# Performance work log

Measured on AMD Instinct MI355X. Metric: run time of the kernel, lower is better.

## Reference

```python
import jax, jax.numpy as jnp
import numpy as np

SMOOTH_COEF = 0.025
FLOOR = 1e-06
B, T, C = 64, 4096, 128


def setup_inputs() -> dict:
    key = jax.random.key(0)
    k1, = jax.random.split(key, 1)
    inputs = jax.random.uniform(k1, (B, T, C), dtype=jnp.float32)  # nonneg spectrogram-like
    alpha = jnp.full((C,), 0.98, dtype=jnp.float32)
    delta = jnp.full((C,), 2.0, dtype=jnp.float32)
    root = jnp.full((C,), 2.0, dtype=jnp.float32)
    return {"inputs": inputs, "alpha": alpha, "delta": delta, "root": root}


def _ema(x, s):
    # m_t = s*x_t + (1-s)*m_{t-1}, with h_{-1} = x_0 => m_0 = x_0.
    # Linear recurrence via associative scan: pairs (a_t, b_t), m_t = a_t*m_{t-1} + b_t.
    Bn, Tn, Cn = x.shape
    a = jnp.full((Tn,), 1.0 - s, dtype=x.dtype).at[0].set(0.0)
    a = jnp.broadcast_to(a[None, :, None], x.shape)
    b = (s * x).at[:, 0, :].set(x[:, 0, :])

    def comb(c1, c2):
        a1, b1 = c1
        a2, b2 = c2
        return (a1 * a2, a2 * b1 + b2)

    _, m = jax.lax.associative_scan(comb, (a, b), axis=1)
    return m


def reference(inputs, alpha, delta, root):
    alpha_c = jnp.minimum(alpha, 1.0)          # [C]
    root_c = jnp.maximum(root, 1.0)            # [C]
    m = _ema(inputs, SMOOTH_COEF)              # [B,T,C] EMA smoother
    one_over_root = 1.0 / root_c
    term1 = jnp.power(FLOOR + m, alpha_c)
    term2 = jnp.power(inputs / term1 + delta, one_over_root)
    term3 = jnp.power(delta, one_over_root)
    return term2 - term3
```

## Files before the change

### kernel.cpp

```cpp
#include <hip/hip_runtime.h>


constexpr int Bn = 64, Tn = 4096, Cn = 128;
constexpr int NC = 64;
constexpr int Lc = Tn / NC;
constexpr float SC  = 0.025f;
constexpr float OMS = 1.0f - SC;
constexpr float FLOORV = 1e-6f;

__host__ __device__ constexpr float chunk_decay() {
    float a = 1.0f;
    for (int i = 0; i < Lc; ++i) a *= OMS;
    return a;
}
constexpr float ACH = chunk_decay();


__global__ __launch_bounds__(256) void k_partial(const float* __restrict__ x,
                                                 float* __restrict__ endv) {
    int gid   = blockIdx.x * 256 + threadIdx.x;
    int cg    = gid & 31;
    int chunk = (gid >> 5) & (NC - 1);
    int b     = gid >> 11;

    const float4* xp = (const float4*)x + (size_t)(b * Tn + chunk * Lc) * (Cn / 4) + cg;

    float4 v = xp[0];
    float4 m;
    if (chunk == 0) {
        m = v;
    } else {
        m.x = SC * v.x; m.y = SC * v.y; m.z = SC * v.z; m.w = SC * v.w;
    }
#pragma unroll 8
    for (int t = 1; t < Lc; ++t) {
        v = xp[(size_t)t * (Cn / 4)];
        m.x = fmaf(OMS, m.x, SC * v.x);
        m.y = fmaf(OMS, m.y, SC * v.y);
        m.z = fmaf(OMS, m.z, SC * v.z);
        m.w = fmaf(OMS, m.w, SC * v.w);
    }
    float4* ep = (float4*)endv + (size_t)(b * NC + chunk) * (Cn / 4) + cg;
    *ep = m;
}

__global__ __launch_bounds__(256) void k_scan(float* __restrict__ endv) {
    int gid = blockIdx.x * 256 + threadIdx.x;
    int cg  = gid & 31;
    int b   = gid >> 5;
    float4* p = (float4*)endv + (size_t)b * NC * (Cn / 4) + cg;
    float4 acc = {0.f, 0.f, 0.f, 0.f};
    for (int j = 0; j < NC; ++j) {
        float4 e = p[(size_t)j * (Cn / 4)];
        p[(size_t)j * (Cn / 4)] = acc;
        acc.x = fmaf(ACH, acc.x, e.x);
        acc.y = fmaf(ACH, acc.y, e.y);
        acc.z = fmaf(ACH, acc.z, e.z);
        acc.w = fmaf(ACH, acc.w, e.w);
    }
}

__device__ __forceinline__ float pcen_elem(float x, float m, float al, float dl,
                                           float oor, float t3) {
    float lg   = log2f(FLOORV + m);
    float inv1 = exp2f(-al * lg);
    float base = fmaf(x, inv1, dl);
    return exp2f(oor * log2f(base)) - t3;
}

__global__ __launch_bounds__(256) void k_final(const float* __restrict__ x,
                                               const float* __restrict__ alpha,
                                               const float* __restrict__ delta,
                                               const float* __restrict__ root,
                                               const float* __restrict__ inc,
                                               float* __restrict__ out) {
    int gid   = blockIdx.x * 256 + threadIdx.x;
    int cg    = gid & 31;
    int chunk = (gid >> 5) & (NC - 1);
    int b     = gid >> 11;
    int c0    = cg * 4;

    float4 al = *(const float4*)(alpha + c0);
    float4 dl = *(const float4*)(delta + c0);
    float4 rt = *(const float4*)(root + c0);
    al.x = fminf(al.x, 1.f); al.y = fminf(al.y, 1.f); al.z = fminf(al.z, 1.f); al.w = fminf(al.w, 1.f);
    rt.x = fmaxf(rt.x, 1.f); rt.y = fmaxf(rt.y, 1.f); rt.z = fmaxf(rt.z, 1.f); rt.w = fmaxf(rt.w, 1.f);
    float4 oor = {1.f / rt.x, 1.f / rt.y, 1.f / rt.z, 1.f / rt.w};
    float4 t3  = {exp2f(oor.x * log2f(dl.x)), exp2f(oor.y * log2f(dl.y)),
                  exp2f(oor.z * log2f(dl.z)), exp2f(oor.w * log2f(dl.w))};

    size_t xoff = (size_t)(b * Tn + chunk * Lc) * (Cn / 4) + cg;
    const float4* xp = (const float4*)x + xoff;
    float4*       op = (float4*)out + xoff;

    float4 m = *((const float4*)inc + (size_t)(b * NC + chunk) * (Cn / 4) + cg);

    float4 v = xp[0];
    if (chunk == 0) {
        m = v;
    } else {
        m.x = fmaf(OMS, m.x, SC * v.x);
        m.y = fmaf(OMS, m.y, SC * v.y);
        m.z = fmaf(OMS, m.z, SC * v.z);
        m.w = fmaf(OMS, m.w, SC * v.w);
    }
    float4 o;
    o.x = pcen_elem(v.x, m.x, al.x, dl.x, oor.x, t3.x);
    o.y = pcen_elem(v.y, m.y, al.y, dl.y, oor.y, t3.y);
    o.z = pcen_elem(v.z, m.z, al.z, dl.z, oor.z, t3.z);
    o.w = pcen_elem(v.w, m.w, al.w, dl.w, oor.w, t3.w);
    op[0] = o;

#pragma unroll 4
    for (int t = 1; t < Lc; ++t) {
        v = xp[(size_t)t * (Cn / 4)];
        m.x = fmaf(OMS, m.x, SC * v.x);
        m.y = fmaf(OMS, m.y, SC * v.y);
        m.z = fmaf(OMS, m.z, SC * v.z);
        m.w = fmaf(OMS, m.w, SC * v.w);
        o.x = pcen_elem(v.x, m.x, al.x, dl.x, oor.x, t3.x);
        o.y = pcen_elem(v.y, m.y, al.y, dl.y, oor.y, t3.y);
        o.z = pcen_elem(v.z, m.z, al.z, dl.z, oor.z, t3.z);
        o.w = pcen_elem(v.w, m.w, al.w, dl.w, oor.w, t3.w);
        op[(size_t)t * (Cn / 4)] = o;
    }
}

extern "C" void kernel_launch(void* const* d_in, const int* in_sizes, int n_in,
                              void* d_out, int out_size, void* d_ws, size_t ws_size,
                              hipStream_t stream) {
    const float* x     = (const float*)d_in[0];
    const float* alpha = (const float*)d_in[1];
    const float* delta = (const float*)d_in[2];
    const float* root  = (const float*)d_in[3];
    float* out = (float*)d_out;
    float* ws  = (float*)d_ws;

    const int total = Bn * NC * (Cn / 4);
    k_partial<<<total / 256, 256, 0, stream>>>(x, ws);
    k_scan<<<(Bn * (Cn / 4)) / 256, 256, 0, stream>>>(ws);
    k_final<<<total / 256, 256, 0, stream>>>(x, alpha, delta, root, ws, out);
}
```

Baseline: 269.4 us.

## Fuse partial, scan and final kernels into one cooperative grid-synced kernel

Replaces the three-kernel chunked EMA pipeline (partial chunk ends, serial carry scan, final PCEN pass) with one cooperative kernel. It writes chunk-end values, does a grid-wide sync, and then has each thread rebuild its own carry-in by scanning all earlier chunk ends. This is meant to remove two kernel-launch boundaries and the separate low-parallelism scan kernel. In exchange it adds a grid barrier, redundant per-thread prefix scans over the workspace, and a co-residency requirement. Launch bounds are raised to allow two blocks per CU so that all 512 blocks can be resident at once.

```diff
diff --git a/kernel.cpp b/kernel.cpp
--- a/kernel.cpp
+++ b/kernel.cpp
@@ -1,4 +1,7 @@
 #include <hip/hip_runtime.h>
+#include <hip/hip_cooperative_groups.h>
+
+namespace cgx = cooperative_groups;
 
 
 constexpr int Bn = 64, Tn = 4096, Cn = 128;
@@ -15,15 +18,32 @@
 }
 constexpr float ACH = chunk_decay();
 
+__device__ __forceinline__ float pcen_elem(float x, float m, float al, float dl,
+                                           float oor, float t3) {
+    float lg   = log2f(FLOORV + m);
+    float inv1 = exp2f(-al * lg);
+    float base = fmaf(x, inv1, dl);
+    return exp2f(oor * log2f(base)) - t3;
+}
 
-__global__ __launch_bounds__(256) void k_partial(const float* __restrict__ x,
-                                                 float* __restrict__ endv) {
-    int gid   = blockIdx.x * 256 + threadIdx.x;
-    int cg    = gid & 31;
-    int chunk = (gid >> 5) & (NC - 1);
-    int b     = gid >> 11;
 
-    const float4* xp = (const float4*)x + (size_t)(b * Tn + chunk * Lc) * (Cn / 4) + cg;
+__global__ __launch_bounds__(256, 2) void k_pcen(
+        const float* __restrict__ x,
+        const float* __restrict__ alpha,
+        const float* __restrict__ delta,
+        const float* __restrict__ root,
+        float* __restrict__ endv,
+        float* __restrict__ out)
+{
+    cgx::grid_group grid = cgx::this_grid();
+
+    const int gid   = blockIdx.x * 256 + threadIdx.x;
+    const int cg    = gid & 31;
+    const int chunk = (gid >> 5) & (NC - 1);
+    const int b     = gid >> 11;
+
+    const size_t xoff = (size_t)(b * Tn + chunk * Lc) * (Cn / 4) + cg;
+    const float4* xp  = (const float4*)x + xoff;
 
     float4 v = xp[0];
     float4 m;
@@ -40,46 +60,24 @@
         m.z = fmaf(OMS, m.z, SC * v.z);
         m.w = fmaf(OMS, m.w, SC * v.w);
     }
-    float4* ep = (float4*)endv + (size_t)(b * NC + chunk) * (Cn / 4) + cg;
-    *ep = m;
-}
+    ((float4*)endv)[(size_t)(b * NC + chunk) * (Cn / 4) + cg] = m;
 
-__global__ __launch_bounds__(256) void k_scan(float* __restrict__ endv) {
-    int gid = blockIdx.x * 256 + threadIdx.x;
-    int cg  = gid & 31;
-    int b   = gid >> 5;
-    float4* p = (float4*)endv + (size_t)b * NC * (Cn / 4) + cg;
+    __threadfence();
+    grid.sync();
+    __threadfence();
+
+    const float4* ep = (const float4*)endv + (size_t)b * NC * (Cn / 4) + cg;
     float4 acc = {0.f, 0.f, 0.f, 0.f};
-    for (int j = 0; j < NC; ++j) {
-        float4 e = p[(size_t)j * (Cn / 4)];
-        p[(size_t)j * (Cn / 4)] = acc;
+#pragma unroll 4
+    for (int j = 0; j < chunk; ++j) {
+        float4 e = ep[(size_t)j * (Cn / 4)];
         acc.x = fmaf(ACH, acc.x, e.x);
         acc.y = fmaf(ACH, acc.y, e.y);
         acc.z = fmaf(ACH, acc.z, e.z);
         acc.w = fmaf(ACH, acc.w, e.w);
     }
-}
 
-__device__ __forceinline__ float pcen_elem(float x, float m, float al, float dl,
-                                           float oor, float t3) {
-    float lg   = log2f(FLOORV + m);
-    float inv1 = exp2f(-al * lg);
-    float base = fmaf(x, inv1, dl);
-    return exp2f(oor * log2f(base)) - t3;
-}
-
-__global__ __launch_bounds__(256) void k_final(const float* __restrict__ x,
-                                               const float* __restrict__ alpha,
-                                               const float* __restrict__ delta,
-                                               const float* __restrict__ root,
-                                               const float* __restrict__ inc,
-                                               float* __restrict__ out) {
-    int gid   = blockIdx.x * 256 + threadIdx.x;
-    int cg    = gid & 31;
-    int chunk = (gid >> 5) & (NC - 1);
-    int b     = gid >> 11;
-    int c0    = cg * 4;
-
+    const int c0 = cg * 4;
     float4 al = *(const float4*)(alpha + c0);
     float4 dl = *(const float4*)(delta + c0);
     float4 rt = *(const float4*)(root + c0);
@@ -89,20 +87,16 @@
     float4 t3  = {exp2f(oor.x * log2f(dl.x)), exp2f(oor.y * log2f(dl.y)),
                   exp2f(oor.z * log2f(dl.z)), exp2f(oor.w * log2f(dl.w))};
 
-    size_t xoff = (size_t)(b * Tn + chunk * Lc) * (Cn / 4) + cg;
-    const float4* xp = (const float4*)x + xoff;
-    float4*       op = (float4*)out + xoff;
+    float4* op = (float4*)out + xoff;
 
-    float4 m = *((const float4*)inc + (size_t)(b * NC + chunk) * (Cn / 4) + cg);
-
-    float4 v = xp[0];
+    v = xp[0];
     if (chunk == 0) {
         m = v;
     } else {
-        m.x = fmaf(OMS, m.x, SC * v.x);
-        m.y = fmaf(OMS, m.y, SC * v.y);
-        m.z = fmaf(OMS, m.z, SC * v.z);
-        m.w = fmaf(OMS, m.w, SC * v.w);
+        m.x = fmaf(OMS, acc.x, SC * v.x);
+        m.y = fmaf(OMS, acc.y, SC * v.y);
+        m.z = fmaf(OMS, acc.z, SC * v.z);
+        m.w = fmaf(OMS, acc.w, SC * v.w);
     }
     float4 o;
     o.x = pcen_elem(v.x, m.x, al.x, dl.x, oor.x, t3.x);
@@ -137,7 +131,8 @@
     float* ws  = (float*)d_ws;
 
     const int total = Bn * NC * (Cn / 4);
-    k_partial<<<total / 256, 256, 0, stream>>>(x, ws);
-    k_scan<<<(Bn * (Cn / 4)) / 256, 256, 0, stream>>>(ws);
-    k_final<<<total / 256, 256, 0, stream>>>(x, alpha, delta, root, ws, out);
+    void* args[] = {(void*)&x, (void*)&alpha, (void*)&delta, (void*)&root,
+                    (void*)&ws, (void*)&out};
+    hipLaunchCooperativeKernel((const void*)k_pcen, dim3(total / 256), dim3(256),
+                               args, 0, stream);
 }
```

Measured after the change: 436.2 us. 1.62x slower.

## Replace chunk scan kernel with windowed prefix recompute and double chunk count

Applied to the files above, without the earlier changes.

Drops the separate serial scan kernel. Each final-pass thread now rebuilds its incoming EMA state from the end values of at most 32 preceding chunks; the truncation relies on the carry decay 0.975^32 per chunk making older chunks numerically negligible. The chunk count is doubled to 128 to expose more parallel threads, and the final loop's unroll factor is raised. The cost is redundant reads of the small end-value buffer and a truncated recurrence with tiny approximation error.

```diff
diff --git a/kernel.cpp b/kernel.cpp
--- a/kernel.cpp
+++ b/kernel.cpp
@@ -2,8 +2,9 @@
 
 
 constexpr int Bn = 64, Tn = 4096, Cn = 128;
-constexpr int NC = 64;
+constexpr int NC = 128;
 constexpr int Lc = Tn / NC;
+constexpr int KWIN = 32;
 constexpr float SC  = 0.025f;
 constexpr float OMS = 1.0f - SC;
 constexpr float FLOORV = 1e-6f;
@@ -21,7 +22,7 @@
     int gid   = blockIdx.x * 256 + threadIdx.x;
     int cg    = gid & 31;
     int chunk = (gid >> 5) & (NC - 1);
-    int b     = gid >> 11;
+    int b     = gid >> 12;
 
     const float4* xp = (const float4*)x + (size_t)(b * Tn + chunk * Lc) * (Cn / 4) + cg;
 
@@ -40,24 +41,7 @@
         m.z = fmaf(OMS, m.z, SC * v.z);
         m.w = fmaf(OMS, m.w, SC * v.w);
     }
-    float4* ep = (float4*)endv + (size_t)(b * NC + chunk) * (Cn / 4) + cg;
-    *ep = m;
-}
-
-__global__ __launch_bounds__(256) void k_scan(float* __restrict__ endv) {
-    int gid = blockIdx.x * 256 + threadIdx.x;
-    int cg  = gid & 31;
-    int b   = gid >> 5;
-    float4* p = (float4*)endv + (size_t)b * NC * (Cn / 4) + cg;
-    float4 acc = {0.f, 0.f, 0.f, 0.f};
-    for (int j = 0; j < NC; ++j) {
-        float4 e = p[(size_t)j * (Cn / 4)];
-        p[(size_t)j * (Cn / 4)] = acc;
-        acc.x = fmaf(ACH, acc.x, e.x);
-        acc.y = fmaf(ACH, acc.y, e.y);
-        acc.z = fmaf(ACH, acc.z, e.z);
-        acc.w = fmaf(ACH, acc.w, e.w);
-    }
+    ((float4*)endv)[(size_t)(b * NC + chunk) * (Cn / 4) + cg] = m;
 }
 
 __device__ __forceinline__ float pcen_elem(float x, float m, float al, float dl,
@@ -72,14 +56,25 @@
                                                const float* __restrict__ alpha,
                                                const float* __restrict__ delta,
                                                const float* __restrict__ root,
-                                               const float* __restrict__ inc,
+                                               const float* __restrict__ endv,
                                                float* __restrict__ out) {
     int gid   = blockIdx.x * 256 + threadIdx.x;
     int cg    = gid & 31;
     int chunk = (gid >> 5) & (NC - 1);
-    int b     = gid >> 11;
-    int c0    = cg * 4;
+    int b     = gid >> 12;
 
+    const float4* ep = (const float4*)endv + (size_t)b * NC * (Cn / 4) + cg;
+    float4 acc = {0.f, 0.f, 0.f, 0.f};
+    int jstart = chunk - KWIN; if (jstart < 0) jstart = 0;
+    for (int j = jstart; j < chunk; ++j) {
+        float4 e = ep[(size_t)j * (Cn / 4)];
+        acc.x = fmaf(ACH, acc.x, e.x);
+        acc.y = fmaf(ACH, acc.y, e.y);
+        acc.z = fmaf(ACH, acc.z, e.z);
+        acc.w = fmaf(ACH, acc.w, e.w);
+    }
+
+    int c0 = cg * 4;
     float4 al = *(const float4*)(alpha + c0);
     float4 dl = *(const float4*)(delta + c0);
     float4 rt = *(const float4*)(root + c0);
@@ -93,16 +88,15 @@
     const float4* xp = (const float4*)x + xoff;
     float4*       op = (float4*)out + xoff;
 
-    float4 m = *((const float4*)inc + (size_t)(b * NC + chunk) * (Cn / 4) + cg);
-
     float4 v = xp[0];
+    float4 m;
     if (chunk == 0) {
         m = v;
     } else {
-        m.x = fmaf(OMS, m.x, SC * v.x);
-        m.y = fmaf(OMS, m.y, SC * v.y);
-        m.z = fmaf(OMS, m.z, SC * v.z);
-        m.w = fmaf(OMS, m.w, SC * v.w);
+        m.x = fmaf(OMS, acc.x, SC * v.x);
+        m.y = fmaf(OMS, acc.y, SC * v.y);
+        m.z = fmaf(OMS, acc.z, SC * v.z);
+        m.w = fmaf(OMS, acc.w, SC * v.w);
     }
     float4 o;
     o.x = pcen_elem(v.x, m.x, al.x, dl.x, oor.x, t3.x);
@@ -111,7 +105,7 @@
     o.w = pcen_elem(v.w, m.w, al.w, dl.w, oor.w, t3.w);
     op[0] = o;
 
-#pragma unroll 4
+#pragma unroll 8
     for (int t = 1; t < Lc; ++t) {
         v = xp[(size_t)t * (Cn / 4)];
         m.x = fmaf(OMS, m.x, SC * v.x);
@@ -138,6 +132,5 @@
 
     const int total = Bn * NC * (Cn / 4);
     k_partial<<<total / 256, 256, 0, stream>>>(x, ws);
-    k_scan<<<(Bn * (Cn / 4)) / 256, 256, 0, stream>>>(ws);
     k_final<<<total / 256, 256, 0, stream>>>(x, alpha, delta, root, ws, out);
 }
```

After: 274.8 us. 1.02x slower.
